# Kernel optimization log

Hardware: AMD Instinct MI355X
Metric: run time of the kernel (lower is better)

The kernel has to match this reference:

```python
import jax, jax.numpy as jnp
import numpy as np

WS = 8          # window size -> N = 64
SHIFT = 4       # shift size for shifted windows
FEAT = 32       # feature map H = W at stage 3
C = 512         # channels (SwinV2-B stage 3)
HEADS = 16
B_IMG = 128     # images -> 128 * (32/8)^2 = 2048 windows


def _rel_coords_table():
    # log-spaced continuous relative coords table, SwinV2 style: [(2W-1)^2, 2]
    r = np.arange(-(WS - 1), WS, dtype=np.float32)
    t = np.stack(np.meshgrid(r, r, indexing='ij'), axis=-1)  # [15,15,2]
    t = t / (WS - 1) * 8.0
    t = np.sign(t) * np.log2(np.abs(t) + 1.0) / np.log2(8.0)
    return t.reshape(-1, 2)


def _rel_pos_index():
    c = np.stack(np.meshgrid(np.arange(WS), np.arange(WS), indexing='ij'))  # [2,8,8]
    cf = c.reshape(2, -1)
    rel = (cf[:, :, None] - cf[:, None, :]).transpose(1, 2, 0)  # [64,64,2]
    rel[:, :, 0] += WS - 1
    rel[:, :, 1] += WS - 1
    rel[:, :, 0] *= 2 * WS - 1
    return rel.sum(-1).astype(np.int32)  # [64,64]


def _shift_mask():
    # standard SwinV2 shifted-window attention mask: [nW, N, N] in {0, -100}
    img = np.zeros((FEAT, FEAT), dtype=np.float32)
    cnt = 0
    for hs in (slice(0, -WS), slice(-WS, -SHIFT), slice(-SHIFT, None)):
        for ws in (slice(0, -WS), slice(-WS, -SHIFT), slice(-SHIFT, None)):
            img[hs, ws] = cnt
            cnt += 1
    win = img.reshape(FEAT // WS, WS, FEAT // WS, WS).transpose(0, 2, 1, 3)
    win = win.reshape(-1, WS * WS)  # [nW, 64]
    diff = win[:, None, :] - win[:, :, None]
    return np.where(diff != 0, -100.0, 0.0).astype(np.float32)


def setup_inputs() -> dict:
    key = jax.random.key(0)
    ks = jax.random.split(key, 10)
    nW = (FEAT // WS) ** 2  # 16 windows per image
    Bw = B_IMG * nW         # 2048
    N = WS * WS
    s = 0.02
    return {
        'x': jax.random.normal(ks[0], (Bw, N, C), jnp.float32),
        'mask': jnp.asarray(_shift_mask()),
        'qkv_w': jax.random.normal(ks[1], (3 * C, C), jnp.float32) * s,
        'q_bias': jnp.zeros((C,), jnp.float32),
        'v_bias': jnp.zeros((C,), jnp.float32),
        'logit_scale': jnp.full((HEADS, 1, 1), np.log(10.0), jnp.float32),
        'cpb_w1': jax.random.normal(ks[2], (512, 2), jnp.float32) * s,
        'cpb_b1': jnp.zeros((512,), jnp.float32),
        'cpb_w2': jax.random.normal(ks[3], (HEADS, 512), jnp.float32) * s,
        'proj_w': jax.random.normal(ks[4], (C, C), jnp.float32) * s,
        'proj_b': jnp.zeros((C,), jnp.float32),
        'rel_coords_table': jnp.asarray(_rel_coords_table()),
        'rel_pos_index': jnp.asarray(_rel_pos_index()),
    }


def reference(x, mask, qkv_w, q_bias, v_bias, logit_scale, cpb_w1, cpb_b1,
              cpb_w2, proj_w, proj_b, rel_coords_table, rel_pos_index):
    Bw, N, Cdim = x.shape
    H = logit_scale.shape[0]
    d = Cdim // H
    # qkv projection; k has no bias (SwinV2)
    qkv_bias = jnp.concatenate([q_bias, jnp.zeros_like(q_bias), v_bias])
    qkv = (x @ qkv_w.T + qkv_bias).reshape(Bw, N, 3, H, d).transpose(2, 0, 3, 1, 4)
    q, k, v = qkv[0], qkv[1], qkv[2]  # each [Bw,H,N,d]
    # cosine attention with learned per-head temperature
    qn = q / jnp.maximum(jnp.linalg.norm(q, axis=-1, keepdims=True), 1e-12)
    kn = k / jnp.maximum(jnp.linalg.norm(k, axis=-1, keepdims=True), 1e-12)
    attn = jnp.einsum('bhnd,bhmd->bhnm', qn, kn)
    scale = jnp.exp(jnp.minimum(logit_scale, jnp.log(100.0)))  # [H,1,1]
    attn = attn * scale[None]
    # continuous relative position bias via small MLP over log-spaced coords
    tbl = jax.nn.relu(rel_coords_table @ cpb_w1.T + cpb_b1) @ cpb_w2.T  # [(2W-1)^2,H]
    bias = tbl[rel_pos_index.reshape(-1)].reshape(N, N, H).transpose(2, 0, 1)
    attn = attn + 16.0 * jax.nn.sigmoid(bias)[None]
    # shifted-window mask applied per window group
    nW = mask.shape[0]
    attn = attn.reshape(Bw // nW, nW, H, N, N) + mask[None, :, None]
    attn = jax.nn.softmax(attn.reshape(Bw, H, N, N), axis=-1)
    out = jnp.einsum('bhnm,bhmd->bhnd', attn, v)
    out = out.transpose(0, 2, 1, 3).reshape(Bw, N, Cdim)
    return out @ proj_w.T + proj_b
```

## Files before the change

### kernel.cpp

```cpp
#include <hip/hip_runtime.h>
#include <stdint.h>
#include <stddef.h>


typedef __attribute__((ext_vector_type(8))) short bf16x8;
typedef __attribute__((ext_vector_type(4))) float f32x4;
typedef __attribute__((ext_vector_type(4))) unsigned short us4;
typedef __attribute__((ext_vector_type(8))) unsigned short us8;
typedef unsigned short u16;
typedef unsigned int u32;

__device__ __forceinline__ u16 f2bf(float f) {
  union { __bf16 b; u16 u; } cv;
  cv.b = (__bf16)f;
  return cv.u;
}
__device__ __forceinline__ float bf2f(u16 s) {
  return __uint_as_float(((u32)s) << 16);
}
__device__ __forceinline__ void gl_lds16(const void* g, void* l) {
  __builtin_amdgcn_global_load_lds(
      (const __attribute__((address_space(1))) u32*)g,
      (__attribute__((address_space(3))) u32*)l, 16, 0, 0);
}
__device__ __forceinline__ f32x4 mfma16(bf16x8 a, bf16x8 b, f32x4 c) {
  return __builtin_amdgcn_mfma_f32_16x16x32_bf16(a, b, c, 0, 0, 0);
}
__device__ __forceinline__ bf16x8 ldswz(const u16* p, int ks) {
  return *(const bf16x8*)((const u16*)((uintptr_t)p ^ (uintptr_t)(ks << 6)));
}


__global__ void conv_w_kernel(const float* __restrict__ QW, const float* __restrict__ PW,
                              u16* __restrict__ WQB, u16* __restrict__ WPB) {
  int idx = blockIdx.x * 256 + threadIdx.x;
  const int NQ = 1536 * 512 / 4;
  float4 v; u16* dst;
  if (idx < NQ) { v = ((const float4*)QW)[idx]; dst = WQB + (size_t)idx * 4; }
  else { int k = idx - NQ; v = ((const float4*)PW)[k]; dst = WPB + (size_t)k * 4; }
  us4 u; u.x = f2bf(v.x); u.y = f2bf(v.y); u.z = f2bf(v.z); u.w = f2bf(v.w);
  *(us4*)dst = u;
}

__global__ void sig16_kernel(const float* __restrict__ CT, const float* __restrict__ W1,
                             const float* __restrict__ B1, const float* __restrict__ W2,
                             float* __restrict__ SIG) {
  int i = blockIdx.x;
  int tid = threadIdx.x;
  float c0 = CT[i * 2 + 0], c1 = CT[i * 2 + 1];
  float a[16];
  #pragma unroll
  for (int hh = 0; hh < 16; ++hh) a[hh] = 0.f;
  #pragma unroll
  for (int jj = 0; jj < 2; ++jj) {
    int j = tid + jj * 256;
    float h = fmaxf(c0 * W1[j * 2 + 0] + c1 * W1[j * 2 + 1] + B1[j], 0.f);
    #pragma unroll
    for (int hh = 0; hh < 16; ++hh) a[hh] += h * W2[hh * 512 + j];
  }
  __shared__ float red[4][16];
  #pragma unroll
  for (int hh = 0; hh < 16; ++hh) {
    float v = a[hh];
    for (int m = 1; m < 64; m <<= 1) v += __shfl_xor(v, m);
    if ((tid & 63) == 0) red[tid >> 6][hh] = v;
  }
  __syncthreads();
  if (tid < 16) {
    float v = red[0][tid] + red[1][tid] + red[2][tid] + red[3][tid];
    SIG[i * 16 + tid] = 16.f / (1.f + __expf(-v));
  }
}

__global__ void cmb_kernel(const float* __restrict__ SIG, const float* __restrict__ MASK,
                           const int* __restrict__ RPI, float* __restrict__ CMB) {
  int b = blockIdx.x;
  int w = b >> 4, h = b & 15;
  int tid = threadIdx.x;
  const float* mrow = &MASK[(size_t)w * 4096];
  float* crow = &CMB[(size_t)b * 4096];
  #pragma unroll
  for (int it = 0; it < 16; ++it) {
    int nm = it * 256 + tid;
    crow[nm] = SIG[RPI[nm] * 16 + h] + mrow[nm];
  }
}


__global__ __launch_bounds__(256, 2) void qkv_gemm(
    const float* __restrict__ X, const u16* __restrict__ WB,
    const float* __restrict__ QB, const float* __restrict__ VB,
    u16* __restrict__ QKV) {
  __shared__ u16 As[128 * 64];
  __shared__ u16 Bs[128 * 64];
  const int tid = threadIdx.x, lane = tid & 63, w = tid >> 6;
  int bid = blockIdx.x;
  int swz = (bid & 7) * 1536 + (bid >> 3);
  const int mt = swz / 12, nt = swz - mt * 12;
  const long m0 = (long)mt * 128, n0 = (long)nt * 128;
  const int wm = w >> 1, wn = w & 1;
  const f32x4 zf = {0.f, 0.f, 0.f, 0.f};

  f32x4 acc[4][4];
  #pragma unroll
  for (int mi = 0; mi < 4; ++mi)
    #pragma unroll
    for (int ni = 0; ni < 4; ++ni) acc[mi][ni] = zf;

  const int fr = lane & 15;
  const int fsw = ((lane >> 4) ^ (lane & 7)) * 8;
  const u16* Ap = &As[(wm * 64 + fr) * 64 + fsw];
  const u16* Bp = &Bs[(wn * 64 + fr) * 64 + fsw];

  for (int t = 0; t < 8; ++t) {
    float4 av[8];
    #pragma unroll
    for (int i = 0; i < 8; ++i) {
      int ch = tid + (i << 8);
      int row = ch >> 4, kc = ch & 15;
      av[i] = *(const float4*)&X[(m0 + row) * 512 + t * 64 + kc * 4];
    }
    #pragma unroll
    for (int i = 0; i < 4; ++i) {
      int ch = ((w << 2) + i) * 64 + lane;
      int row = ch >> 3, kc = (ch & 7) ^ (row & 7);
      gl_lds16(&WB[(n0 + row) * 512 + t * 64 + kc * 8], &Bs[((w << 2) + i) * 512]);
    }
    #pragma unroll
    for (int i = 0; i < 8; ++i) {
      int ch = tid + (i << 8);
      int row = ch >> 4, kc = ch & 15;
      int kcs = kc ^ ((row & 7) << 1);
      us4 u; u.x = f2bf(av[i].x); u.y = f2bf(av[i].y); u.z = f2bf(av[i].z); u.w = f2bf(av[i].w);
      *(us4*)&As[row * 64 + kcs * 4] = u;
    }
    __syncthreads();
    #pragma unroll
    for (int ks = 0; ks < 2; ++ks) {
      bf16x8 af[4], bfr[4];
      #pragma unroll
      for (int mi = 0; mi < 4; ++mi) af[mi] = ldswz(Ap + mi * 1024, ks);
      #pragma unroll
      for (int ni = 0; ni < 4; ++ni) bfr[ni] = ldswz(Bp + ni * 1024, ks);
      #pragma unroll
      for (int mi = 0; mi < 4; ++mi)
        #pragma unroll
        for (int ni = 0; ni < 4; ++ni)
          acc[mi][ni] = mfma16(af[mi], bfr[ni], acc[mi][ni]);
    }
    __syncthreads();
  }

  #pragma unroll
  for (int ni = 0; ni < 4; ++ni) {
    const long c = n0 + wn * 64 + ni * 16 + (lane & 15);
    float bias = (c < 512) ? QB[c] : (c < 1024 ? 0.f : VB[c - 1024]);
    #pragma unroll
    for (int mi = 0; mi < 4; ++mi)
      #pragma unroll
      for (int r = 0; r < 4; ++r) {
        long row = m0 + wm * 64 + mi * 16 + (lane >> 4) * 4 + r;
        QKV[row * 1536 + c] = f2bf(acc[mi][ni][r] + bias);
      }
  }
}


__global__ __launch_bounds__(256, 4) void attn_kernel(
    u16* __restrict__ QKV, const float* __restrict__ CMB, const float* __restrict__ LS) {
  __shared__ u16 sm[7424];
  u16* qs = sm;
  u16* ksm = sm + 2560;
  u16* ps = sm;
  u16* vt = sm + 5120;
  const int tid = threadIdx.x, lane = tid & 63, w = tid >> 6;
  const int b = blockIdx.x, wi = b & 15;
  const size_t base = (size_t)b * 64 * 1536;
  const int cl = lane & 15, lg = lane >> 4;
  const int srow = tid >> 2, sck = tid & 3;
  const int vd = tid & 31, vkb = tid >> 5;
  const f32x4 zf = {0.f, 0.f, 0.f, 0.f};

  for (int h = 0; h < 16; ++h) {
    const float scale = __expf(fminf(LS[h], 4.6051702f));
    {
      us8 qv = *(const us8*)&QKV[base + (size_t)srow * 1536 + h * 32 + sck * 8];
      float qf[8]; float ss = 0.f;
      #pragma unroll
      for (int j = 0; j < 8; ++j) { qf[j] = bf2f(qv[j]); ss += qf[j] * qf[j]; }
      ss += __shfl_xor(ss, 1); ss += __shfl_xor(ss, 2);
      float rn = scale / fmaxf(sqrtf(ss), 1e-12f);
      us8 qo;
      #pragma unroll
      for (int j = 0; j < 8; ++j) qo[j] = f2bf(qf[j] * rn);
      *(us8*)&qs[srow * 40 + sck * 8] = qo;
    }
    {
      us8 kv = *(const us8*)&QKV[base + (size_t)srow * 1536 + 512 + h * 32 + sck * 8];
      float kf[8]; float ss = 0.f;
      #pragma unroll
      for (int j = 0; j < 8; ++j) { kf[j] = bf2f(kv[j]); ss += kf[j] * kf[j]; }
      ss += __shfl_xor(ss, 1); ss += __shfl_xor(ss, 2);
      float rn = 1.f / fmaxf(sqrtf(ss), 1e-12f);
      us8 ko;
      #pragma unroll
      for (int j = 0; j < 8; ++j) ko[j] = f2bf(kf[j] * rn);
      *(us8*)&ksm[srow * 40 + sck * 8] = ko;
    }
    {
      us8 vo;
      #pragma unroll
      for (int e = 0; e < 8; ++e)
        vo[e] = QKV[base + (size_t)(vkb * 8 + e) * 1536 + 1024 + h * 32 + vd];
      *(us8*)&vt[vd * 72 + vkb * 8] = vo;
    }
    __syncthreads();

    bf16x8 aq = *(const bf16x8*)&qs[(w * 16 + cl) * 40 + lg * 8];
    f32x4 s4[4];
    #pragma unroll
    for (int nt = 0; nt < 4; ++nt) {
      bf16x8 bk = *(const bf16x8*)&ksm[(nt * 16 + cl) * 40 + lg * 8];
      s4[nt] = mfma16(aq, bk, zf);
    }

    const float* cp = &CMB[((size_t)(wi * 16 + h)) << 12];
    const int r0 = w * 16 + lg * 4;
    float p[4][4];
    #pragma unroll
    for (int r = 0; r < 4; ++r) {
      float mx = -3.0e38f;
      #pragma unroll
      for (int q4 = 0; q4 < 4; ++q4) {
        float v = s4[q4][r] + cp[(r0 + r) * 64 + q4 * 16 + cl];
        p[q4][r] = v; mx = fmaxf(mx, v);
      }
      mx = fmaxf(mx, __shfl_xor(mx, 1));
      mx = fmaxf(mx, __shfl_xor(mx, 2));
      mx = fmaxf(mx, __shfl_xor(mx, 4));
      mx = fmaxf(mx, __shfl_xor(mx, 8));
      float sum = 0.f;
      #pragma unroll
      for (int q4 = 0; q4 < 4; ++q4) { float e = __expf(p[q4][r] - mx); p[q4][r] = e; sum += e; }
      sum += __shfl_xor(sum, 1); sum += __shfl_xor(sum, 2);
      sum += __shfl_xor(sum, 4); sum += __shfl_xor(sum, 8);
      float inv = 1.f / sum;
      #pragma unroll
      for (int q4 = 0; q4 < 4; ++q4) p[q4][r] *= inv;
    }
    __syncthreads();

    #pragma unroll
    for (int r = 0; r < 4; ++r)
      #pragma unroll
      for (int q4 = 0; q4 < 4; ++q4)
        ps[(r0 + r) * 72 + q4 * 16 + cl] = f2bf(p[q4][r]);

    f32x4 o4[2]; o4[0] = zf; o4[1] = zf;
    #pragma unroll
    for (int ks = 0; ks < 2; ++ks) {
      bf16x8 ap = *(const bf16x8*)&ps[(w * 16 + cl) * 72 + ks * 32 + lg * 8];
      #pragma unroll
      for (int n2 = 0; n2 < 2; ++n2) {
        bf16x8 bv = *(const bf16x8*)&vt[(n2 * 16 + cl) * 72 + ks * 32 + lg * 8];
        o4[n2] = mfma16(ap, bv, o4[n2]);
      }
    }
    #pragma unroll
    for (int n2 = 0; n2 < 2; ++n2)
      #pragma unroll
      for (int r = 0; r < 4; ++r)
        QKV[base + (size_t)(w * 16 + lg * 4 + r) * 1536 + h * 32 + n2 * 16 + cl] = f2bf(o4[n2][r]);
    __syncthreads();
  }
}


__global__ __launch_bounds__(256, 2) void proj_gemm(
    const u16* __restrict__ A, const u16* __restrict__ WB,
    const float* __restrict__ PB, float* __restrict__ OUT) {
  __shared__ u16 As[128 * 64];
  __shared__ u16 Bs[128 * 64];
  const int tid = threadIdx.x, lane = tid & 63, w = tid >> 6;
  int bid = blockIdx.x;
  int swz = (bid & 7) * 512 + (bid >> 3);
  const int mt = swz >> 2, nt = swz & 3;
  const long m0 = (long)mt * 128, n0 = (long)nt * 128;
  const int wm = w >> 1, wn = w & 1;
  const f32x4 zf = {0.f, 0.f, 0.f, 0.f};

  f32x4 acc[4][4];
  #pragma unroll
  for (int mi = 0; mi < 4; ++mi)
    #pragma unroll
    for (int ni = 0; ni < 4; ++ni) acc[mi][ni] = zf;

  const int fr = lane & 15;
  const int fsw = ((lane >> 4) ^ (lane & 7)) * 8;
  const u16* Ap = &As[(wm * 64 + fr) * 64 + fsw];
  const u16* Bp = &Bs[(wn * 64 + fr) * 64 + fsw];

  for (int t = 0; t < 8; ++t) {
    #pragma unroll
    for (int i = 0; i < 4; ++i) {
      int ch = ((w << 2) + i) * 64 + lane;
      int row = ch >> 3, kc = (ch & 7) ^ (row & 7);
      gl_lds16(&A[(m0 + row) * 1536 + t * 64 + kc * 8], &As[((w << 2) + i) * 512]);
      gl_lds16(&WB[(n0 + row) * 512 + t * 64 + kc * 8], &Bs[((w << 2) + i) * 512]);
    }
    __syncthreads();
    #pragma unroll
    for (int ks = 0; ks < 2; ++ks) {
      bf16x8 af[4], bfr[4];
      #pragma unroll
      for (int mi = 0; mi < 4; ++mi) af[mi] = ldswz(Ap + mi * 1024, ks);
      #pragma unroll
      for (int ni = 0; ni < 4; ++ni) bfr[ni] = ldswz(Bp + ni * 1024, ks);
      #pragma unroll
      for (int mi = 0; mi < 4; ++mi)
        #pragma unroll
        for (int ni = 0; ni < 4; ++ni)
          acc[mi][ni] = mfma16(af[mi], bfr[ni], acc[mi][ni]);
    }
    __syncthreads();
  }

  #pragma unroll
  for (int ni = 0; ni < 4; ++ni) {
    const long c = n0 + wn * 64 + ni * 16 + (lane & 15);
    float bias = PB[c];
    #pragma unroll
    for (int mi = 0; mi < 4; ++mi)
      #pragma unroll
      for (int r = 0; r < 4; ++r) {
        long row = m0 + wm * 64 + mi * 16 + (lane >> 4) * 4 + r;
        OUT[row * 512 + c] = acc[mi][ni][r] + bias;
      }
  }
}


extern "C" void kernel_launch(void* const* d_in, const int* in_sizes, int n_in,
                              void* d_out, int out_size, void* d_ws, size_t ws_size,
                              hipStream_t stream) {
  const float* X    = (const float*)d_in[0];
  const float* MASK = (const float*)d_in[1];
  const float* QW   = (const float*)d_in[2];
  const float* QB   = (const float*)d_in[3];
  const float* VB   = (const float*)d_in[4];
  const float* LS   = (const float*)d_in[5];
  const float* CW1  = (const float*)d_in[6];
  const float* CB1  = (const float*)d_in[7];
  const float* CW2  = (const float*)d_in[8];
  const float* PW   = (const float*)d_in[9];
  const float* PB   = (const float*)d_in[10];
  const float* CT   = (const float*)d_in[11];
  const int*   RPI  = (const int*)d_in[12];
  float* OUT = (float*)d_out;

  char* ws = (char*)d_ws;
  u16*   QKV = (u16*)ws;
  float* CMB = (float*)(ws + 402653184ull);
  float* SIG = (float*)(ws + 406847488ull);
  u16*   WQB = (u16*)(ws + 406861888ull);
  u16*   WPB = (u16*)(ws + 408434752ull);

  conv_w_kernel<<<1024, 256, 0, stream>>>(QW, PW, WQB, WPB);
  sig16_kernel<<<225, 256, 0, stream>>>(CT, CW1, CB1, CW2, SIG);
  cmb_kernel<<<256, 256, 0, stream>>>(SIG, MASK, RPI, CMB);
  qkv_gemm<<<12288, 256, 0, stream>>>(X, WQB, QB, VB, QKV);
  attn_kernel<<<2048, 256, 0, stream>>>(QKV, CMB, LS);
  proj_gemm<<<4096, 256, 0, stream>>>(QKV, WPB, PB, OUT);
}
```

Baseline: 753.8 us.

## Pre-convert X to bf16 and use a 256x256 pipelined QKV GEMM

Adds a kernel that converts the fp32 input X to bf16 in workspace, then runs a new QKV GEMM with 256x256 tiles, 512 threads, and double-buffered direct global-to-LDS loads. Explicit waitcnt, barriers and setprio interleave the loads with the MFMA work. The aim is more data reuse per tile and less register-staged conversion inside the GEMM. The cost is an extra full pass over X (read 268MB fp32, write 134MB bf16), and the path is used only when the workspace is large enough, otherwise it falls back to the old kernel.

After: 824.1 us. +9.3%, slower.

```diff
diff --git a/kernel.cpp b/kernel.cpp
--- a/kernel.cpp
+++ b/kernel.cpp
@@ -9,6 +9,11 @@
 typedef __attribute__((ext_vector_type(8))) unsigned short us8;
 typedef unsigned short u16;
 typedef unsigned int u32;
+
+#define FENCE() asm volatile("" ::: "memory")
+#define WAITV4() asm volatile("s_waitcnt vmcnt(4)" ::: "memory")
+#define WAITV0() asm volatile("s_waitcnt vmcnt(0)" ::: "memory")
+#define WAITL0() asm volatile("s_waitcnt lgkmcnt(0)" ::: "memory")
 
 __device__ __forceinline__ u16 f2bf(float f) {
   union { __bf16 b; u16 u; } cv;
@@ -42,6 +47,16 @@
   *(us4*)dst = u;
 }
 
+__global__ void xconv_kernel(const float* __restrict__ X, u16* __restrict__ XB) {
+  size_t idx = (size_t)blockIdx.x * 256 + threadIdx.x;
+  float4 a = ((const float4*)X)[idx * 2];
+  float4 b = ((const float4*)X)[idx * 2 + 1];
+  us8 o;
+  o[0] = f2bf(a.x); o[1] = f2bf(a.y); o[2] = f2bf(a.z); o[3] = f2bf(a.w);
+  o[4] = f2bf(b.x); o[5] = f2bf(b.y); o[6] = f2bf(b.z); o[7] = f2bf(b.w);
+  *(us8*)&XB[idx * 8] = o;
+}
+
 __global__ void sig16_kernel(const float* __restrict__ CT, const float* __restrict__ W1,
                              const float* __restrict__ B1, const float* __restrict__ W2,
                              float* __restrict__ SIG) {
@@ -87,7 +102,109 @@
 }
 
 
-__global__ __launch_bounds__(256, 2) void qkv_gemm(
+__global__ __launch_bounds__(512, 1) void qkv_gemm8(
+    const u16* __restrict__ XB, const u16* __restrict__ WB,
+    const float* __restrict__ QB, const float* __restrict__ VB,
+    u16* __restrict__ QKV) {
+  __shared__ u16 S[65536];
+  const int tid = threadIdx.x, lane = tid & 63, w = tid >> 6;
+  int bid = blockIdx.x;
+  int swz = (bid & 7) * 384 + (bid >> 3);
+  const int mt = swz / 6, nt = swz - mt * 6;
+  const long m0 = (long)mt * 256, n0 = (long)nt * 256;
+  const int wm = w >> 2, wn = w & 3;
+  const int fr = lane & 15, lg = lane >> 4;
+  const int fsw = (lg ^ (lane & 7)) << 3;
+  const f32x4 zf = {0.f, 0.f, 0.f, 0.f};
+
+  f32x4 acc[8][4];
+  #pragma unroll
+  for (int mi = 0; mi < 8; ++mi)
+    #pragma unroll
+    for (int ni = 0; ni < 4; ++ni) acc[mi][ni] = zf;
+
+  auto stageA = [&](int kt, int h) {
+    int dst = (kt & 1) * 32768 + h * 8192;
+    #pragma unroll
+    for (int i = 0; i < 2; ++i) {
+      int ch = i * 512 + tid;
+      int row = ch >> 3, kcs = (ch & 7) ^ (row & 7);
+      gl_lds16(&XB[(size_t)(m0 + h * 128 + row) * 512 + kt * 64 + kcs * 8],
+               &S[dst + (i * 512 + w * 64) * 8]);
+    }
+  };
+  auto stageB = [&](int kt, int h) {
+    int dst = (kt & 1) * 32768 + 16384 + h * 8192;
+    #pragma unroll
+    for (int i = 0; i < 2; ++i) {
+      int ch = i * 512 + tid;
+      int row = ch >> 3, kcs = (ch & 7) ^ (row & 7);
+      gl_lds16(&WB[(size_t)(n0 + h * 128 + row) * 512 + kt * 64 + kcs * 8],
+               &S[dst + (i * 512 + w * 64) * 8]);
+    }
+  };
+
+  stageA(0, 0); stageB(0, 0); stageB(0, 1); stageA(0, 1);
+  stageA(1, 0); stageB(1, 0);
+  WAITV4();
+  FENCE(); __builtin_amdgcn_s_barrier(); FENCE();
+
+  for (int t = 0; t < 8; ++t) {
+    const int buf = (t & 1) * 32768;
+    #pragma unroll
+    for (int p = 0; p < 4; ++p) {
+      const int qm = p >> 1, qn = p & 1;
+      bf16x8 af0[4], af1[4], bv0[2], bv1[2];
+      #pragma unroll
+      for (int m = 0; m < 4; ++m) {
+        const u16* pA = &S[buf + (qm * 128 + wm * 64 + m * 16 + fr) * 64 + fsw];
+        af0[m] = ldswz(pA, 0);
+        af1[m] = ldswz(pA, 1);
+      }
+      #pragma unroll
+      for (int n = 0; n < 2; ++n) {
+        const u16* pB = &S[buf + 16384 + (qn * 128 + wn * 32 + n * 16 + fr) * 64 + fsw];
+        bv0[n] = ldswz(pB, 0);
+        bv1[n] = ldswz(pB, 1);
+      }
+      if (p == 0)      { if (t < 7) stageB(t + 1, 1); }
+      else if (p == 1) { if (t < 7) stageA(t + 1, 1); }
+      else if (p == 2) { if (t < 6) stageA(t + 2, 0); }
+      else {
+        if (t < 6) { stageB(t + 2, 0); WAITV4(); }
+        else if (t == 6) { WAITV0(); }
+      }
+      FENCE(); __builtin_amdgcn_s_barrier(); FENCE();
+      WAITL0(); __builtin_amdgcn_sched_barrier(0);
+      __builtin_amdgcn_s_setprio(1);
+      #pragma unroll
+      for (int m = 0; m < 4; ++m)
+        #pragma unroll
+        for (int n = 0; n < 2; ++n) {
+          acc[qm * 4 + m][qn * 2 + n] = mfma16(af0[m], bv0[n], acc[qm * 4 + m][qn * 2 + n]);
+          acc[qm * 4 + m][qn * 2 + n] = mfma16(af1[m], bv1[n], acc[qm * 4 + m][qn * 2 + n]);
+        }
+      __builtin_amdgcn_s_setprio(0);
+      FENCE(); __builtin_amdgcn_s_barrier(); FENCE();
+    }
+  }
+
+  #pragma unroll
+  for (int ni = 0; ni < 4; ++ni) {
+    const long c = n0 + (ni >> 1) * 128 + wn * 32 + (ni & 1) * 16 + fr;
+    float bias = (c < 512) ? QB[c] : (c < 1024 ? 0.f : VB[c - 1024]);
+    #pragma unroll
+    for (int mi = 0; mi < 8; ++mi)
+      #pragma unroll
+      for (int r = 0; r < 4; ++r) {
+        long row = m0 + (mi >> 2) * 128 + wm * 64 + (mi & 3) * 16 + lg * 4 + r;
+        QKV[row * 1536 + c] = f2bf(acc[mi][ni][r] + bias);
+      }
+  }
+}
+
+
+__global__ __launch_bounds__(256, 2) void qkv_gemm_rs(
     const float* __restrict__ X, const u16* __restrict__ WB,
     const float* __restrict__ QB, const float* __restrict__ VB,
     u16* __restrict__ QKV) {
@@ -327,7 +444,7 @@
 
   #pragma unroll
   for (int ni = 0; ni < 4; ++ni) {
-    const long c = n0 + wn * 64 + ni * 16 + (lane & 15);
+    const long c = n0 + wn * 64 + ni * 16 + fr;
     float bias = PB[c];
     #pragma unroll
     for (int mi = 0; mi < 4; ++mi)
@@ -359,16 +476,24 @@
   float* OUT = (float*)d_out;
 
   char* ws = (char*)d_ws;
-  u16*   QKV = (u16*)ws;
-  float* CMB = (float*)(ws + 402653184ull);
-  float* SIG = (float*)(ws + 406847488ull);
-  u16*   WQB = (u16*)(ws + 406861888ull);
-  u16*   WPB = (u16*)(ws + 408434752ull);
+  const bool big = ws_size >= 543178752ull;
+  u16* QKV = (u16*)ws;
+  u16* XB  = (u16*)(ws + 402653184ull);
+  size_t off = big ? 536870912ull : 402653184ull;
+  float* CMB = (float*)(ws + off);  off += 4194304ull;
+  float* SIG = (float*)(ws + off);  off += 16384ull;
+  u16*   WQB = (u16*)(ws + off);    off += 1572864ull;
+  u16*   WPB = (u16*)(ws + off);
 
   conv_w_kernel<<<1024, 256, 0, stream>>>(QW, PW, WQB, WPB);
   sig16_kernel<<<225, 256, 0, stream>>>(CT, CW1, CB1, CW2, SIG);
   cmb_kernel<<<256, 256, 0, stream>>>(SIG, MASK, RPI, CMB);
-  qkv_gemm<<<12288, 256, 0, stream>>>(X, WQB, QB, VB, QKV);
+  if (big) {
+    xconv_kernel<<<32768, 256, 0, stream>>>(X, XB);
+    qkv_gemm8<<<3072, 512, 0, stream>>>(XB, WQB, QB, VB, QKV);
+  } else {
+    qkv_gemm_rs<<<12288, 256, 0, stream>>>(X, WQB, QB, VB, QKV);
+  }
   attn_kernel<<<2048, 256, 0, stream>>>(QKV, CMB, LS);
   proj_gemm<<<4096, 256, 0, stream>>>(QKV, WPB, PB, OUT);
 }
```

## Add triple-buffered 128x256 GEMM kernels with bf16 pre-converted X

Applied to the files above, without the earlier changes.

Replaces the QKV and projection GEMMs with 512-thread kernels using 128x256 tiles, a three-stage LDS ring with explicit vmcnt waits, split barriers and setprio around the MFMA blocks. When the workspace is large enough, X is first converted to bf16 by a separate pass so the QKV GEMM can stream bf16 directly via global_load_lds. The aim is to hide global-load latency and cut per-iteration sync overhead. The cost is an extra full read and write of X, plus a workspace-size dependent code path.

After: 680.7 us. -9.7%, faster.

```diff
diff --git a/kernel.cpp b/kernel.cpp
--- a/kernel.cpp
+++ b/kernel.cpp
@@ -9,6 +9,12 @@
 typedef __attribute__((ext_vector_type(8))) unsigned short us8;
 typedef unsigned short u16;
 typedef unsigned int u32;
+
+#define FENCE() asm volatile("" ::: "memory")
+#define WAITV4() asm volatile("s_waitcnt vmcnt(4)" ::: "memory")
+#define WAITV3() asm volatile("s_waitcnt vmcnt(3)" ::: "memory")
+#define WAITV0() asm volatile("s_waitcnt vmcnt(0)" ::: "memory")
+#define WAITL0() asm volatile("s_waitcnt lgkmcnt(0)" ::: "memory")
 
 __device__ __forceinline__ u16 f2bf(float f) {
   union { __bf16 b; u16 u; } cv;
@@ -42,6 +48,16 @@
   *(us4*)dst = u;
 }
 
+__global__ void xconv_kernel(const float* __restrict__ X, u16* __restrict__ XB) {
+  size_t idx = (size_t)blockIdx.x * 256 + threadIdx.x;
+  float4 a = ((const float4*)X)[idx * 2];
+  float4 b = ((const float4*)X)[idx * 2 + 1];
+  us8 o;
+  o[0] = f2bf(a.x); o[1] = f2bf(a.y); o[2] = f2bf(a.z); o[3] = f2bf(a.w);
+  o[4] = f2bf(b.x); o[5] = f2bf(b.y); o[6] = f2bf(b.z); o[7] = f2bf(b.w);
+  *(us8*)&XB[idx * 8] = o;
+}
+
 __global__ void sig16_kernel(const float* __restrict__ CT, const float* __restrict__ W1,
                              const float* __restrict__ B1, const float* __restrict__ W2,
                              float* __restrict__ SIG) {
@@ -87,7 +103,163 @@
 }
 
 
-__global__ __launch_bounds__(256, 2) void qkv_gemm(
+#define GEMM32_KLOOP()                                                     \
+  _Pragma("unroll")                                                        \
+  for (int t = 0; t < 16; ++t) {                                           \
+    const int Sb = (t % 3) * 12288;                                        \
+    _Pragma("unroll")                                                      \
+    for (int m = 0; m < 4; ++m)                                            \
+      af[m] = *(const bf16x8*)&S[Sb + (wm * 64 + m * 16 + fr) * 32 + fsw]; \
+    _Pragma("unroll")                                                      \
+    for (int n = 0; n < 2; ++n)                                            \
+      bf[n] = *(const bf16x8*)&S[Sb + 4096 + (wn * 64 + n * 16 + fr) * 32 + fsw]; \
+    if (t + 2 <= 15) stageB(t + 2);                                        \
+    FENCE(); __builtin_amdgcn_s_barrier(); FENCE();                        \
+    WAITL0(); __builtin_amdgcn_sched_barrier(0);                           \
+    __builtin_amdgcn_s_setprio(1);                                         \
+    _Pragma("unroll")                                                      \
+    for (int m = 0; m < 4; ++m)                                            \
+      _Pragma("unroll")                                                    \
+      for (int n = 0; n < 2; ++n)                                          \
+        acc[m][n] = mfma16(af[m], bf[n], acc[m][n]);                       \
+    __builtin_amdgcn_s_setprio(0);                                         \
+    FENCE(); __builtin_amdgcn_s_barrier(); FENCE();                        \
+    _Pragma("unroll")                                                      \
+    for (int n = 0; n < 2; ++n)                                            \
+      bf[n] = *(const bf16x8*)&S[Sb + 4096 + (wn * 64 + (n + 2) * 16 + fr) * 32 + fsw]; \
+    if (t + 3 <= 15) stageA(t + 3);                                        \
+    if (t <= 12) { WAITV4(); }                                             \
+    else if (t == 13) { WAITV3(); }                                        \
+    else if (t == 14) { WAITV0(); }                                        \
+    FENCE(); __builtin_amdgcn_s_barrier(); FENCE();                        \
+    WAITL0(); __builtin_amdgcn_sched_barrier(0);                           \
+    __builtin_amdgcn_s_setprio(1);                                         \
+    _Pragma("unroll")                                                      \
+    for (int m = 0; m < 4; ++m)                                            \
+      _Pragma("unroll")                                                    \
+      for (int n = 0; n < 2; ++n)                                          \
+        acc[m][n + 2] = mfma16(af[m], bf[n], acc[m][n + 2]);               \
+    __builtin_amdgcn_s_setprio(0);                                         \
+    FENCE(); __builtin_amdgcn_s_barrier(); FENCE();                        \
+  }
+
+
+__global__ __launch_bounds__(512, 4) void qkv_g32(
+    const u16* __restrict__ XB, const u16* __restrict__ WB,
+    const float* __restrict__ QB, const float* __restrict__ VB,
+    u16* __restrict__ QKV) {
+  __shared__ u16 S[36864];
+  const int tid = threadIdx.x, lane = tid & 63, w = tid >> 6;
+  int bid = blockIdx.x;
+  int swz = (bid & 7) * 768 + (bid >> 3);
+  const int mt = swz / 6, nt = swz - mt * 6;
+  const long m0 = (long)mt * 128, n0 = (long)nt * 256;
+  const int wm = w >> 2, wn = w & 3;
+  const int fr = lane & 15, lg = lane >> 4;
+  const int fsw = (lg ^ (lane & 3)) << 3;
+  const f32x4 zf = {0.f, 0.f, 0.f, 0.f};
+
+  f32x4 acc[4][4];
+  #pragma unroll
+  for (int mi = 0; mi < 4; ++mi)
+    #pragma unroll
+    for (int ni = 0; ni < 4; ++ni) acc[mi][ni] = zf;
+
+  const int arow = tid >> 2;
+  const int asc = (tid & 3) ^ (arow & 3);
+  const u16* aSrc = &XB[(size_t)(m0 + arow) * 512 + asc * 8];
+  const u16* bSrc0 = &WB[(size_t)(n0 + arow) * 512 + asc * 8];
+  const u16* bSrc1 = &WB[(size_t)(n0 + 128 + arow) * 512 + asc * 8];
+
+  auto stageA = [&](int kt) {
+    gl_lds16(aSrc + kt * 32, &S[(kt % 3) * 12288 + w * 512]);
+  };
+  auto stageB = [&](int kt) {
+    gl_lds16(bSrc0 + kt * 32, &S[(kt % 3) * 12288 + 4096 + w * 512]);
+    gl_lds16(bSrc1 + kt * 32, &S[(kt % 3) * 12288 + 8192 + w * 512]);
+  };
+
+  bf16x8 af[4], bf[2];
+
+  stageA(0); stageB(0); stageA(1); stageB(1); stageA(2);
+  WAITV4();
+  FENCE(); __builtin_amdgcn_s_barrier(); FENCE();
+
+  GEMM32_KLOOP()
+
+  #pragma unroll
+  for (int ni = 0; ni < 4; ++ni) {
+    const long c = n0 + wn * 64 + ni * 16 + fr;
+    float bias = (c < 512) ? QB[c] : (c < 1024 ? 0.f : VB[c - 1024]);
+    #pragma unroll
+    for (int mi = 0; mi < 4; ++mi)
+      #pragma unroll
+      for (int r = 0; r < 4; ++r) {
+        long row = m0 + wm * 64 + mi * 16 + lg * 4 + r;
+        QKV[row * 1536 + c] = f2bf(acc[mi][ni][r] + bias);
+      }
+  }
+}
+
+
+__global__ __launch_bounds__(512, 4) void proj_g32(
+    const u16* __restrict__ A, const u16* __restrict__ WB,
+    const float* __restrict__ PB, float* __restrict__ OUT) {
+  __shared__ u16 S[36864];
+  const int tid = threadIdx.x, lane = tid & 63, w = tid >> 6;
+  int bid = blockIdx.x;
+  int swz = (bid & 7) * 256 + (bid >> 3);
+  const int mt = swz >> 1, nt = swz & 1;
+  const long m0 = (long)mt * 128, n0 = (long)nt * 256;
+  const int wm = w >> 2, wn = w & 3;
+  const int fr = lane & 15, lg = lane >> 4;
+  const int fsw = (lg ^ (lane & 3)) << 3;
+  const f32x4 zf = {0.f, 0.f, 0.f, 0.f};
+
+  f32x4 acc[4][4];
+  #pragma unroll
+  for (int mi = 0; mi < 4; ++mi)
+    #pragma unroll
+    for (int ni = 0; ni < 4; ++ni) acc[mi][ni] = zf;
+
+  const int arow = tid >> 2;
+  const int asc = (tid & 3) ^ (arow & 3);
+  const u16* aSrc = &A[(size_t)(m0 + arow) * 1536 + asc * 8];
+  const u16* bSrc0 = &WB[(size_t)(n0 + arow) * 512 + asc * 8];
+  const u16* bSrc1 = &WB[(size_t)(n0 + 128 + arow) * 512 + asc * 8];
+
+  auto stageA = [&](int kt) {
+    gl_lds16(aSrc + kt * 32, &S[(kt % 3) * 12288 + w * 512]);
+  };
+  auto stageB = [&](int kt) {
+    gl_lds16(bSrc0 + kt * 32, &S[(kt % 3) * 12288 + 4096 + w * 512]);
+    gl_lds16(bSrc1 + kt * 32, &S[(kt % 3) * 12288 + 8192 + w * 512]);
+  };
+
+  bf16x8 af[4], bf[2];
+
+  stageA(0); stageB(0); stageA(1); stageB(1); stageA(2);
+  WAITV4();
+  FENCE(); __builtin_amdgcn_s_barrier(); FENCE();
+
+  GEMM32_KLOOP()
+
+  #pragma unroll
+  for (int ni = 0; ni < 4; ++ni) {
+    const long c = n0 + wn * 64 + ni * 16 + fr;
+    float bias = PB[c];
+    #pragma unroll
+    for (int mi = 0; mi < 4; ++mi)
+      #pragma unroll
+      for (int r = 0; r < 4; ++r) {
+        long row = m0 + wm * 64 + mi * 16 + lg * 4 + r;
+        OUT[row * 512 + c] = acc[mi][ni][r] + bias;
+      }
+  }
+}
+
+
+__global__ __launch_bounds__(256, 2) void qkv_gemm_rs(
     const float* __restrict__ X, const u16* __restrict__ WB,
     const float* __restrict__ QB, const float* __restrict__ VB,
     u16* __restrict__ QKV) {
@@ -272,70 +444,6 @@
       for (int r = 0; r < 4; ++r)
         QKV[base + (size_t)(w * 16 + lg * 4 + r) * 1536 + h * 32 + n2 * 16 + cl] = f2bf(o4[n2][r]);
     __syncthreads();
-  }
-}
-
-
-__global__ __launch_bounds__(256, 2) void proj_gemm(
-    const u16* __restrict__ A, const u16* __restrict__ WB,
-    const float* __restrict__ PB, float* __restrict__ OUT) {
-  __shared__ u16 As[128 * 64];
-  __shared__ u16 Bs[128 * 64];
-  const int tid = threadIdx.x, lane = tid & 63, w = tid >> 6;
-  int bid = blockIdx.x;
-  int swz = (bid & 7) * 512 + (bid >> 3);
-  const int mt = swz >> 2, nt = swz & 3;
-  const long m0 = (long)mt * 128, n0 = (long)nt * 128;
-  const int wm = w >> 1, wn = w & 1;
-  const f32x4 zf = {0.f, 0.f, 0.f, 0.f};
-
-  f32x4 acc[4][4];
-  #pragma unroll
-  for (int mi = 0; mi < 4; ++mi)
-    #pragma unroll
-    for (int ni = 0; ni < 4; ++ni) acc[mi][ni] = zf;
-
-  const int fr = lane & 15;
-  const int fsw = ((lane >> 4) ^ (lane & 7)) * 8;
-  const u16* Ap = &As[(wm * 64 + fr) * 64 + fsw];
-  const u16* Bp = &Bs[(wn * 64 + fr) * 64 + fsw];
-
-  for (int t = 0; t < 8; ++t) {
-    #pragma unroll
-    for (int i = 0; i < 4; ++i) {
-      int ch = ((w << 2) + i) * 64 + lane;
-      int row = ch >> 3, kc = (ch & 7) ^ (row & 7);
-      gl_lds16(&A[(m0 + row) * 1536 + t * 64 + kc * 8], &As[((w << 2) + i) * 512]);
-      gl_lds16(&WB[(n0 + row) * 512 + t * 64 + kc * 8], &Bs[((w << 2) + i) * 512]);
-    }
-    __syncthreads();
-    #pragma unroll
-    for (int ks = 0; ks < 2; ++ks) {
-      bf16x8 af[4], bfr[4];
-      #pragma unroll
-      for (int mi = 0; mi < 4; ++mi) af[mi] = ldswz(Ap + mi * 1024, ks);
-      #pragma unroll
-      for (int ni = 0; ni < 4; ++ni) bfr[ni] = ldswz(Bp + ni * 1024, ks);
-      #pragma unroll
-      for (int mi = 0; mi < 4; ++mi)
-        #pragma unroll
-        for (int ni = 0; ni < 4; ++ni)
-          acc[mi][ni] = mfma16(af[mi], bfr[ni], acc[mi][ni]);
-    }
-    __syncthreads();
-  }
-
-  #pragma unroll
-  for (int ni = 0; ni < 4; ++ni) {
-    const long c = n0 + wn * 64 + ni * 16 + (lane & 15);
-    float bias = PB[c];
-    #pragma unroll
-    for (int mi = 0; mi < 4; ++mi)
-      #pragma unroll
-      for (int r = 0; r < 4; ++r) {
-        long row = m0 + wm * 64 + mi * 16 + (lane >> 4) * 4 + r;
-        OUT[row * 512 + c] = acc[mi][ni][r] + bias;
-      }
   }
 }
 
@@ -359,16 +467,24 @@
   float* OUT = (float*)d_out;
 
   char* ws = (char*)d_ws;
-  u16*   QKV = (u16*)ws;
-  float* CMB = (float*)(ws + 402653184ull);
-  float* SIG = (float*)(ws + 406847488ull);
-  u16*   WQB = (u16*)(ws + 406861888ull);
-  u16*   WPB = (u16*)(ws + 408434752ull);
+  const bool big = ws_size >= 543178752ull;
+  u16* QKV = (u16*)ws;
+  u16* XB  = (u16*)(ws + 402653184ull);
+  size_t off = big ? 536870912ull : 402653184ull;
+  float* CMB = (float*)(ws + off);  off += 4194304ull;
+  float* SIG = (float*)(ws + off);  off += 16384ull;
+  u16*   WQB = (u16*)(ws + off);    off += 1572864ull;
+  u16*   WPB = (u16*)(ws + off);
 
   conv_w_kernel<<<1024, 256, 0, stream>>>(QW, PW, WQB, WPB);
   sig16_kernel<<<225, 256, 0, stream>>>(CT, CW1, CB1, CW2, SIG);
   cmb_kernel<<<256, 256, 0, stream>>>(SIG, MASK, RPI, CMB);
-  qkv_gemm<<<12288, 256, 0, stream>>>(X, WQB, QB, VB, QKV);
+  if (big) {
+    xconv_kernel<<<32768, 256, 0, stream>>>(X, XB);
+    qkv_g32<<<6144, 512, 0, stream>>>(XB, WQB, QB, VB, QKV);
+  } else {
+    qkv_gemm_rs<<<12288, 256, 0, stream>>>(X, WQB, QB, VB, QKV);
+  }
   attn_kernel<<<2048, 256, 0, stream>>>(QKV, CMB, LS);
-  proj_gemm<<<4096, 256, 0, stream>>>(QKV, WPB, PB, OUT);
-}
+  proj_g32<<<2048, 512, 0, stream>>>(QKV, WPB, PB, OUT);
+}
```
